# Optimization experiments

Measured on AMD Instinct MI355X. Metric: run time of the kernel, lower is better.

Reference implementation:

```python
import jax, jax.numpy as jnp
import numpy as np

BUCKET_SIZE = 128
HEADS = 8
HEAD_DIM = 64
LOOK_BACKWARD = 1
LOOK_FORWARD = 0  # causal => no look forward
TOKEN_SELF_ATTN_VALUE = -50000.0


def look_around(x, backward, forward, pad_value):
    n = x.shape[1]
    pw = [(0, 0)] * x.ndim
    pw[1] = (backward, forward)
    px = jnp.pad(x, pw, constant_values=pad_value)
    return jnp.concatenate([px[:, i:i + n] for i in range(backward + forward + 1)], axis=2)


def shift(x):
    # relative-shift trick: (..., i, j) -> (..., i, j)
    *lead, i, j = x.shape
    x = jnp.concatenate([x, jnp.zeros((*lead, i, i), x.dtype)], axis=-1)
    l = i + j - 1
    x = x.reshape(*lead, i * (i + j))
    pad = (-x.shape[-1]) % l
    x = jnp.concatenate([x, jnp.zeros((*lead, pad), x.dtype)], axis=-1)
    x = x.reshape(*lead, -1, l)
    return x[..., :i, i - 1:]


def setup_inputs() -> dict:
    key = jax.random.key(0)
    kq, kk, kv, kr = jax.random.split(key, 4)
    B, H, T, E = 2, HEADS, 8192, HEAD_DIM
    q = jax.random.normal(kq, (B, H, T, E), dtype=jnp.float32)
    k = jax.random.normal(kk, (B, H, T, E), dtype=jnp.float32)
    v = jax.random.normal(kv, (B, H, T, E), dtype=jnp.float32)
    rel_weights = jax.random.normal(kr, (2 * BUCKET_SIZE, H, E), dtype=jnp.float32)
    return {"q": q, "k": k, "v": v, "rel_weights": rel_weights}


def reference(q, k, v, rel_weights):
    B, H, T, E = q.shape
    qm = q.reshape(B * H, T, E)
    km = k.reshape(B * H, T, E)
    vm = v.reshape(B * H, T, E)

    # shared_qk: l2-normalize keys (F.normalize with eps=1e-12)
    km = km / jnp.maximum(jnp.linalg.norm(km, axis=-1, keepdims=True), 1e-12)

    buckets = T // BUCKET_SIZE
    bq = qm.reshape(B * H, buckets, BUCKET_SIZE, E)
    bk = km.reshape(B * H, buckets, BUCKET_SIZE, E)
    bv = vm.reshape(B * H, buckets, BUCKET_SIZE, E)

    bk = look_around(bk, LOOK_BACKWARD, LOOK_FORWARD, -1.0)
    bv = look_around(bv, LOOK_BACKWARD, LOOK_FORWARD, -1.0)

    ticker = jnp.arange(T, dtype=q.dtype)
    bq_t = ticker.reshape(1, buckets, BUCKET_SIZE)
    bq_k = look_around(bq_t, LOOK_BACKWARD, LOOK_FORWARD, -1.0)

    scale = E ** -0.5
    dots = jnp.einsum('bnie,bnje->bnij', bq, bk) * scale

    # relative positional bias
    bq5 = bq.reshape(B, H, buckets, BUCKET_SIZE, E)
    emb = jnp.einsum('bhnid,jhd->bhnij', bq5, rel_weights) * scale
    dots = dots + shift(emb).reshape(dots.shape)

    mask_value = -jnp.finfo(dots.dtype).max
    # shared_qk: mask self-attention positions
    self_mask = bq_t[:, :, :, None] == bq_k[:, :, None, :]
    dots = jnp.where(self_mask, TOKEN_SELF_ATTN_VALUE, dots)
    # causal mask
    causal_mask = bq_t[:, :, :, None] < bq_k[:, :, None, :]
    dots = jnp.where(causal_mask, mask_value, dots)
    # look-around padding mask
    pad_mask = (bq_k == -1.0)[:, :, None, :]
    dots = jnp.where(pad_mask, mask_value, dots)

    attn = jax.nn.softmax(dots, axis=-1)
    out = jnp.einsum('bnij,bnje->bnie', attn, bv)
    return out.reshape(B, H, T, E)
```

## Files before the change

kernel.cpp:

```cpp
#include <hip/hip_runtime.h>
#include <float.h>

#define NHEAD 8

typedef __attribute__((ext_vector_type(8))) short bf16x8;
typedef __attribute__((ext_vector_type(4))) float f32x4;

static __device__ __forceinline__ unsigned short bfbits(float f) {
    unsigned int u = __float_as_uint(f);
    u += 0x7fffu + ((u >> 16) & 1u);
    return (unsigned short)(u >> 16);
}
static __device__ __forceinline__ float bf2f_lo(unsigned int u) { return __uint_as_float(u << 16); }
static __device__ __forceinline__ float bf2f_hi(unsigned int u) { return __uint_as_float(u & 0xffff0000u); }

static __device__ __forceinline__ int swz64(int r, int c) {
    return (r << 6) + (c ^ ((r & 7) << 3));
}
static __device__ __forceinline__ int vIdx(int c, int kk) {
    return (c << 8) + (kk ^ ((c & 31) << 2));
}
static __device__ __forceinline__ int pIdx(int wv, int row, int col) {
    const int ch = (col >> 3) ^ (row & 3);
    return (wv * 16 + row) * 40 + ch * 8 + (col & 7);
}

static __device__ __forceinline__ f32x4 mfma16(bf16x8 a, bf16x8 b, f32x4 c) {
    return __builtin_amdgcn_mfma_f32_16x16x32_bf16(a, b, c, 0, 0, 0);
}

__global__ __launch_bounds__(512, 4)
void local_attn_kernel(const float* __restrict__ qg, const float* __restrict__ kg,
                       const float* __restrict__ vg, const float* __restrict__ rwg,
                       float* __restrict__ outg)
{
    __shared__ __align__(16) unsigned short sB[256 * 64];
    __shared__ __align__(16) unsigned short sV[64 * 256];
    __shared__ __align__(16) unsigned short sP[8 * 16 * 40];

    const int tid  = threadIdx.x;
    const int lane = tid & 63;
    const int wv   = tid >> 6;
    const int jl   = lane & 15;
    const int hi   = lane >> 4;

    const int lb = ((blockIdx.x & 7) << 7) + (blockIdx.x >> 3);
    const int bh = lb >> 6;
    const int n  = lb & 63;
    const int h  = bh & 7;

    const float scale = 0.125f;

    const float* Qp = qg + ((size_t)bh * 8192 + (size_t)n * 128) * 64;
    const float* Kp = kg + (size_t)bh * 8192 * 64 + ((long)n - 1) * 128 * 64;
    const float* Vp = vg + (size_t)bh * 8192 * 64 + ((long)n - 1) * 128 * 64;

    const int cr = tid >> 4;
    const int c0 = (tid & 15) << 2;

    #pragma unroll
    for (int pp = 0; pp < 8; ++pp) {
        const int row = pp * 32 + cr;
        f32x4 x = {0.f, 0.f, 0.f, 0.f};
        if (!(n == 0 && row < 128))
            x = *reinterpret_cast<const f32x4*>(Vp + row * 64 + c0);
        #pragma unroll
        for (int q = 0; q < 4; ++q)
            sV[vIdx(c0 + q, row)] = bfbits(x[q]);
    }

    const int arow = wv * 16 + jl;
    const int kq0  = hi << 3;
    const float* qr = Qp + arow * 64 + kq0;
    const f32x4 qa = *reinterpret_cast<const f32x4*>(qr);
    const f32x4 qb = *reinterpret_cast<const f32x4*>(qr + 4);
    const f32x4 qc = *reinterpret_cast<const f32x4*>(qr + 32);
    const f32x4 qd = *reinterpret_cast<const f32x4*>(qr + 36);
    bf16x8 aq0, aq1;
    #pragma unroll
    for (int q = 0; q < 4; ++q) {
        aq0[q]     = (short)bfbits(qa[q] * scale);
        aq0[q + 4] = (short)bfbits(qb[q] * scale);
        aq1[q]     = (short)bfbits(qc[q] * scale);
        aq1[q + 4] = (short)bfbits(qd[q] * scale);
    }

    #pragma unroll
    for (int pp = 0; pp < 8; ++pp) {
        const int row = pp * 32 + cr;
        const f32x4 x = *reinterpret_cast<const f32x4*>(rwg + ((size_t)row * NHEAD + h) * 64 + c0);
        ushort4 pk = make_ushort4(bfbits(x[0]), bfbits(x[1]), bfbits(x[2]), bfbits(x[3]));
        *reinterpret_cast<ushort4*>(&sB[swz64(row, c0)]) = pk;
    }

    f32x4 kreg[8];
    #pragma unroll
    for (int pp = 0; pp < 8; ++pp) {
        const int row = pp * 32 + cr;
        if (n == 0 && row < 128) kreg[pp] = f32x4{0.f, 0.f, 0.f, 0.f};
        else kreg[pp] = *reinterpret_cast<const f32x4*>(Kp + row * 64 + c0);
    }

    __syncthreads();

    const int ibase = wv * 16 + (hi << 2);

    unsigned int e01[17], e23[17];
    #pragma unroll
    for (int s = 0; s < 17; ++s) {
        unsigned int p01 = 0, p23 = 0;
        const int ts = s + 7 - wv;
        if (ts >= 0 && ts < 16) {
            const int rr = ts * 16 + jl;
            const bf16x8 b0 = *reinterpret_cast<const bf16x8*>(&sB[swz64(rr, kq0)]);
            const bf16x8 b1 = *reinterpret_cast<const bf16x8*>(&sB[swz64(rr, 32 + kq0)]);
            f32x4 e = {0.f, 0.f, 0.f, 0.f};
            e = mfma16(aq0, b0, e);
            e = mfma16(aq1, b1, e);
            p01 = (unsigned int)bfbits(e[0]) | ((unsigned int)bfbits(e[1]) << 16);
            p23 = (unsigned int)bfbits(e[2]) | ((unsigned int)bfbits(e[3]) << 16);
        }
        e01[s] = p01; e23[s] = p23;
    }

    __syncthreads();

    #pragma unroll
    for (int pp = 0; pp < 8; ++pp) {
        const int row = pp * 32 + cr;
        const f32x4 x = kreg[pp];
        float ss = x[0] * x[0] + x[1] * x[1] + x[2] * x[2] + x[3] * x[3];
        ss += __shfl_xor(ss, 1);
        ss += __shfl_xor(ss, 2);
        ss += __shfl_xor(ss, 4);
        ss += __shfl_xor(ss, 8);
        const float rn = 1.0f / fmaxf(sqrtf(ss), 1e-12f);
        ushort4 pk = make_ushort4(bfbits(x[0] * rn), bfbits(x[1] * rn),
                                  bfbits(x[2] * rn), bfbits(x[3] * rn));
        *reinterpret_cast<ushort4*>(&sB[swz64(row, c0)]) = pk;
    }

    __syncthreads();

    const int tMax = wv + 8;
    const int cv0 = 4 * hi + 1, cv1 = 4 * hi + 2, cv2 = 4 * hi + 3, cv3 = 4 * hi + 4;
    const int sl0 = (hi << 4) | ((jl - cv0) & 15);
    const int sl1 = (hi << 4) | ((jl - cv1) & 15);
    const int sl2 = (hi << 4) | ((jl - cv2) & 15);
    const int sl3 = (hi << 4) | ((jl - cv3) & 15);
    const bool g0 = jl >= cv0, g1 = jl >= cv1, g2 = jl >= cv2, g3 = jl >= cv3;

    unsigned int lo0 = (unsigned int)__shfl((int)e01[0], sl0);
    unsigned int lo1 = (unsigned int)__shfl((int)e01[0], sl1);
    unsigned int lo2 = (unsigned int)__shfl((int)e23[0], sl2);
    unsigned int lo3 = (unsigned int)__shfl((int)e23[0], sl3);

    f32x4 dots[16] = {};
    #pragma unroll
    for (int t = 0; t < 16; ++t) {
        if (t <= tMax) {
            const unsigned int h0 = (unsigned int)__shfl((int)e01[t + 1], sl0);
            const unsigned int h1 = (unsigned int)__shfl((int)e01[t + 1], sl1);
            const unsigned int h2 = (unsigned int)__shfl((int)e23[t + 1], sl2);
            const unsigned int h3 = (unsigned int)__shfl((int)e23[t + 1], sl3);
            const int rr = t * 16 + jl;
            const bf16x8 b0 = *reinterpret_cast<const bf16x8*>(&sB[swz64(rr, kq0)]);
            const bf16x8 b1 = *reinterpret_cast<const bf16x8*>(&sB[swz64(rr, 32 + kq0)]);
            f32x4 d = {0.f, 0.f, 0.f, 0.f};
            d = mfma16(aq0, b0, d);
            d = mfma16(aq1, b1, d);
            const float bias[4] = { bf2f_lo(g0 ? h0 : lo0), bf2f_hi(g1 ? h1 : lo1),
                                    bf2f_lo(g2 ? h2 : lo2), bf2f_hi(g3 ? h3 : lo3) };
            #pragma unroll
            for (int r = 0; r < 4; ++r) {
                const int i  = ibase + r;
                const int dd = rr - i;
                float x = d[r] + bias[r];
                x = (dd == 128) ? -50000.0f : x;
                x = (dd > 128) ? -3.0e38f : x;
                if (n == 0) x = (rr < 128) ? -3.0e38f : x;
                d[r] = x;
            }
            dots[t] = d;
            lo0 = h0; lo1 = h1; lo2 = h2; lo3 = h3;
        }
    }

    float mx[4] = {-3.0e38f, -3.0e38f, -3.0e38f, -3.0e38f};
    #pragma unroll
    for (int t = 0; t < 16; ++t) {
        if (t <= tMax) {
            #pragma unroll
            for (int r = 0; r < 4; ++r) mx[r] = fmaxf(mx[r], dots[t][r]);
        }
    }
    #pragma unroll
    for (int r = 0; r < 4; ++r) {
        mx[r] = fmaxf(mx[r], __shfl_xor(mx[r], 1));
        mx[r] = fmaxf(mx[r], __shfl_xor(mx[r], 2));
        mx[r] = fmaxf(mx[r], __shfl_xor(mx[r], 4));
        mx[r] = fmaxf(mx[r], __shfl_xor(mx[r], 8));
    }
    float sm[4] = {0.f, 0.f, 0.f, 0.f};
    #pragma unroll
    for (int t = 0; t < 16; ++t) {
        if (t <= tMax) {
            #pragma unroll
            for (int r = 0; r < 4; ++r) {
                const float pe = __expf(dots[t][r] - mx[r]);
                dots[t][r] = pe;
                sm[r] += pe;
            }
        }
    }
    float rinv[4];
    #pragma unroll
    for (int r = 0; r < 4; ++r) {
        sm[r] += __shfl_xor(sm[r], 1);
        sm[r] += __shfl_xor(sm[r], 2);
        sm[r] += __shfl_xor(sm[r], 4);
        sm[r] += __shfl_xor(sm[r], 8);
        rinv[r] = 1.0f / sm[r];
    }

    f32x4 o[4] = {};
    #pragma unroll
    for (int pv = 0; pv < 8; ++pv) {
        if (2 * pv <= tMax) {
            #pragma unroll
            for (int tt = 0; tt < 2; ++tt) {
                const int t = 2 * pv + tt;
                #pragma unroll
                for (int r = 0; r < 4; ++r) {
                    unsigned short val = 0;
                    if (t <= tMax) val = bfbits(dots[t][r]);
                    sP[pIdx(wv, 4 * hi + r, tt * 16 + jl)] = val;
                }
            }
            const bf16x8 pa = *reinterpret_cast<const bf16x8*>(&sP[pIdx(wv, jl, kq0)]);
            #pragma unroll
            for (int ct = 0; ct < 4; ++ct) {
                const int c = ct * 16 + jl;
                const ushort4 v0 = *reinterpret_cast<const ushort4*>(&sV[vIdx(c, pv * 32 + kq0)]);
                const ushort4 v1 = *reinterpret_cast<const ushort4*>(&sV[vIdx(c, pv * 32 + kq0 + 4)]);
                bf16x8 vb;
                vb[0] = (short)v0.x; vb[1] = (short)v0.y; vb[2] = (short)v0.z; vb[3] = (short)v0.w;
                vb[4] = (short)v1.x; vb[5] = (short)v1.y; vb[6] = (short)v1.z; vb[7] = (short)v1.w;
                o[ct] = mfma16(pa, vb, o[ct]);
            }
        }
    }

    float* Op = outg + ((size_t)bh * 8192 + (size_t)n * 128) * 64;
    #pragma unroll
    for (int ct = 0; ct < 4; ++ct)
        #pragma unroll
        for (int r = 0; r < 4; ++r)
            Op[(ibase + r) * 64 + ct * 16 + jl] = o[ct][r] * rinv[r];
}

extern "C" void kernel_launch(void* const* d_in, const int* in_sizes, int n_in,
                              void* d_out, int out_size, void* d_ws, size_t ws_size,
                              hipStream_t stream) {
    const float* q  = (const float*)d_in[0];
    const float* k  = (const float*)d_in[1];
    const float* v  = (const float*)d_in[2];
    const float* rw = (const float*)d_in[3];
    float* out = (float*)d_out;
    local_attn_kernel<<<dim3(1024), dim3(512), 0, stream>>>(q, k, v, rw, out);
}
```

Measured before the change: 59.68 us.

## Reorder phases: compute QK first, then interleave rel-bias MFMA with shifts

The kernel now normalizes K into shared memory first and computes the QK dot products before loading the relative-position weights. The relative-bias MFMAs are computed on the fly inside the masking loop rather than stored in two 17-entry register arrays. The f32 K register staging array is replaced by a smaller packed bf16 rel-weight array. It also switches to the library bf16 conversion intrinsic and uses a bit_cast to build V fragments, cutting register pressure and conversion ALU work at the cost of restructured phase ordering.

```diff
diff --git a/kernel.cpp b/kernel.cpp
--- a/kernel.cpp
+++ b/kernel.cpp
@@ -1,4 +1,5 @@
 #include <hip/hip_runtime.h>
+#include <hip/hip_bf16.h>
 #include <float.h>
 
 #define NHEAD 8
@@ -6,10 +7,14 @@
 typedef __attribute__((ext_vector_type(8))) short bf16x8;
 typedef __attribute__((ext_vector_type(4))) float f32x4;
 
-static __device__ __forceinline__ unsigned short bfbits(float f) {
-    unsigned int u = __float_as_uint(f);
-    u += 0x7fffu + ((u >> 16) & 1u);
-    return (unsigned short)(u >> 16);
+struct US44 { ushort4 a, b; };
+
+static __device__ __forceinline__ unsigned short bfb(float f) {
+    __hip_bfloat16 h = __float2bfloat16(f);
+    unsigned short u; __builtin_memcpy(&u, &h, 2); return u;
+}
+static __device__ __forceinline__ unsigned int pk2(float a, float b) {
+    return (unsigned int)bfb(a) | ((unsigned int)bfb(b) << 16);
 }
 static __device__ __forceinline__ float bf2f_lo(unsigned int u) { return __uint_as_float(u << 16); }
 static __device__ __forceinline__ float bf2f_hi(unsigned int u) { return __uint_as_float(u & 0xffff0000u); }
@@ -66,8 +71,36 @@
             x = *reinterpret_cast<const f32x4*>(Vp + row * 64 + c0);
         #pragma unroll
         for (int q = 0; q < 4; ++q)
-            sV[vIdx(c0 + q, row)] = bfbits(x[q]);
-    }
+            sV[vIdx(c0 + q, row)] = bfb(x[q]);
+    }
+
+    #pragma unroll
+    for (int pp = 0; pp < 8; ++pp) {
+        const int row = pp * 32 + cr;
+        f32x4 x = {0.f, 0.f, 0.f, 0.f};
+        if (!(n == 0 && row < 128))
+            x = *reinterpret_cast<const f32x4*>(Kp + row * 64 + c0);
+        float ss = x[0] * x[0] + x[1] * x[1] + x[2] * x[2] + x[3] * x[3];
+        ss += __shfl_xor(ss, 1);
+        ss += __shfl_xor(ss, 2);
+        ss += __shfl_xor(ss, 4);
+        ss += __shfl_xor(ss, 8);
+        const float rn = 1.0f / fmaxf(sqrtf(ss), 1e-12f);
+        ushort4 pkk = make_ushort4(bfb(x[0] * rn), bfb(x[1] * rn),
+                                   bfb(x[2] * rn), bfb(x[3] * rn));
+        *reinterpret_cast<ushort4*>(&sB[swz64(row, c0)]) = pkk;
+    }
+
+    uint2 rwu[8];
+    #pragma unroll
+    for (int pp = 0; pp < 8; ++pp) {
+        const int row = pp * 32 + cr;
+        const f32x4 x = *reinterpret_cast<const f32x4*>(rwg + ((size_t)row * NHEAD + h) * 64 + c0);
+        rwu[pp] = make_uint2(pk2(x[0], x[1]), pk2(x[2], x[3]));
+    }
+    #pragma unroll
+    for (int pp = 0; pp < 8; ++pp)
+        asm volatile("" :: "v"(rwu[pp].x), "v"(rwu[pp].y));
 
     const int arow = wv * 16 + jl;
     const int kq0  = hi << 3;
@@ -79,48 +112,29 @@
     bf16x8 aq0, aq1;
     #pragma unroll
     for (int q = 0; q < 4; ++q) {
-        aq0[q]     = (short)bfbits(qa[q] * scale);
-        aq0[q + 4] = (short)bfbits(qb[q] * scale);
-        aq1[q]     = (short)bfbits(qc[q] * scale);
-        aq1[q + 4] = (short)bfbits(qd[q] * scale);
-    }
-
-    #pragma unroll
-    for (int pp = 0; pp < 8; ++pp) {
-        const int row = pp * 32 + cr;
-        const f32x4 x = *reinterpret_cast<const f32x4*>(rwg + ((size_t)row * NHEAD + h) * 64 + c0);
-        ushort4 pk = make_ushort4(bfbits(x[0]), bfbits(x[1]), bfbits(x[2]), bfbits(x[3]));
-        *reinterpret_cast<ushort4*>(&sB[swz64(row, c0)]) = pk;
-    }
-
-    f32x4 kreg[8];
-    #pragma unroll
-    for (int pp = 0; pp < 8; ++pp) {
-        const int row = pp * 32 + cr;
-        if (n == 0 && row < 128) kreg[pp] = f32x4{0.f, 0.f, 0.f, 0.f};
-        else kreg[pp] = *reinterpret_cast<const f32x4*>(Kp + row * 64 + c0);
+        aq0[q]     = (short)bfb(qa[q] * scale);
+        aq0[q + 4] = (short)bfb(qb[q] * scale);
+        aq1[q]     = (short)bfb(qc[q] * scale);
+        aq1[q + 4] = (short)bfb(qd[q] * scale);
     }
 
     __syncthreads();
 
     const int ibase = wv * 16 + (hi << 2);
-
-    unsigned int e01[17], e23[17];
-    #pragma unroll
-    for (int s = 0; s < 17; ++s) {
-        unsigned int p01 = 0, p23 = 0;
-        const int ts = s + 7 - wv;
-        if (ts >= 0 && ts < 16) {
-            const int rr = ts * 16 + jl;
+    const int tMax  = wv + 8;
+
+    f32x4 dots[16] = {};
+    #pragma unroll
+    for (int t = 0; t < 16; ++t) {
+        if (t <= tMax) {
+            const int rr = t * 16 + jl;
             const bf16x8 b0 = *reinterpret_cast<const bf16x8*>(&sB[swz64(rr, kq0)]);
             const bf16x8 b1 = *reinterpret_cast<const bf16x8*>(&sB[swz64(rr, 32 + kq0)]);
-            f32x4 e = {0.f, 0.f, 0.f, 0.f};
-            e = mfma16(aq0, b0, e);
-            e = mfma16(aq1, b1, e);
-            p01 = (unsigned int)bfbits(e[0]) | ((unsigned int)bfbits(e[1]) << 16);
-            p23 = (unsigned int)bfbits(e[2]) | ((unsigned int)bfbits(e[3]) << 16);
-        }
-        e01[s] = p01; e23[s] = p23;
+            f32x4 d = {0.f, 0.f, 0.f, 0.f};
+            d = mfma16(aq0, b0, d);
+            d = mfma16(aq1, b1, d);
+            dots[t] = d;
+        }
     }
 
     __syncthreads();
@@ -128,21 +142,11 @@
     #pragma unroll
     for (int pp = 0; pp < 8; ++pp) {
         const int row = pp * 32 + cr;
-        const f32x4 x = kreg[pp];
-        float ss = x[0] * x[0] + x[1] * x[1] + x[2] * x[2] + x[3] * x[3];
-        ss += __shfl_xor(ss, 1);
-        ss += __shfl_xor(ss, 2);
-        ss += __shfl_xor(ss, 4);
-        ss += __shfl_xor(ss, 8);
-        const float rn = 1.0f / fmaxf(sqrtf(ss), 1e-12f);
-        ushort4 pk = make_ushort4(bfbits(x[0] * rn), bfbits(x[1] * rn),
-                                  bfbits(x[2] * rn), bfbits(x[3] * rn));
-        *reinterpret_cast<ushort4*>(&sB[swz64(row, c0)]) = pk;
+        *reinterpret_cast<uint2*>(&sB[swz64(row, c0)]) = rwu[pp];
     }
 
     __syncthreads();
 
-    const int tMax = wv + 8;
     const int cv0 = 4 * hi + 1, cv1 = 4 * hi + 2, cv2 = 4 * hi + 3, cv3 = 4 * hi + 4;
     const int sl0 = (hi << 4) | ((jl - cv0) & 15);
     const int sl1 = (hi << 4) | ((jl - cv1) & 15);
@@ -150,38 +154,54 @@
     const int sl3 = (hi << 4) | ((jl - cv3) & 15);
     const bool g0 = jl >= cv0, g1 = jl >= cv1, g2 = jl >= cv2, g3 = jl >= cv3;
 
-    unsigned int lo0 = (unsigned int)__shfl((int)e01[0], sl0);
-    unsigned int lo1 = (unsigned int)__shfl((int)e01[0], sl1);
-    unsigned int lo2 = (unsigned int)__shfl((int)e23[0], sl2);
-    unsigned int lo3 = (unsigned int)__shfl((int)e23[0], sl3);
-
-    f32x4 dots[16] = {};
-    #pragma unroll
-    for (int t = 0; t < 16; ++t) {
-        if (t <= tMax) {
-            const unsigned int h0 = (unsigned int)__shfl((int)e01[t + 1], sl0);
-            const unsigned int h1 = (unsigned int)__shfl((int)e01[t + 1], sl1);
-            const unsigned int h2 = (unsigned int)__shfl((int)e23[t + 1], sl2);
-            const unsigned int h3 = (unsigned int)__shfl((int)e23[t + 1], sl3);
-            const int rr = t * 16 + jl;
-            const bf16x8 b0 = *reinterpret_cast<const bf16x8*>(&sB[swz64(rr, kq0)]);
-            const bf16x8 b1 = *reinterpret_cast<const bf16x8*>(&sB[swz64(rr, 32 + kq0)]);
-            f32x4 d = {0.f, 0.f, 0.f, 0.f};
-            d = mfma16(aq0, b0, d);
-            d = mfma16(aq1, b1, d);
+    unsigned int cur01, cur23;
+    {
+        const int rr = (7 - wv) * 16 + jl;
+        const bf16x8 b0 = *reinterpret_cast<const bf16x8*>(&sB[swz64(rr, kq0)]);
+        const bf16x8 b1 = *reinterpret_cast<const bf16x8*>(&sB[swz64(rr, 32 + kq0)]);
+        f32x4 e = {0.f, 0.f, 0.f, 0.f};
+        e = mfma16(aq0, b0, e);
+        e = mfma16(aq1, b1, e);
+        cur01 = pk2(e[0], e[1]);
+        cur23 = pk2(e[2], e[3]);
+    }
+    unsigned int lo0 = (unsigned int)__shfl((int)cur01, sl0);
+    unsigned int lo1 = (unsigned int)__shfl((int)cur01, sl1);
+    unsigned int lo2 = (unsigned int)__shfl((int)cur23, sl2);
+    unsigned int lo3 = (unsigned int)__shfl((int)cur23, sl3);
+
+    #pragma unroll
+    for (int t = 0; t < 16; ++t) {
+        if (t <= tMax) {
+            unsigned int n01 = 0, n23 = 0;
+            const int ts = t + 8 - wv;
+            if (ts < 16) {
+                const int rr = ts * 16 + jl;
+                const bf16x8 b0 = *reinterpret_cast<const bf16x8*>(&sB[swz64(rr, kq0)]);
+                const bf16x8 b1 = *reinterpret_cast<const bf16x8*>(&sB[swz64(rr, 32 + kq0)]);
+                f32x4 e = {0.f, 0.f, 0.f, 0.f};
+                e = mfma16(aq0, b0, e);
+                e = mfma16(aq1, b1, e);
+                n01 = pk2(e[0], e[1]);
+                n23 = pk2(e[2], e[3]);
+            }
+            const unsigned int h0 = (unsigned int)__shfl((int)n01, sl0);
+            const unsigned int h1 = (unsigned int)__shfl((int)n01, sl1);
+            const unsigned int h2 = (unsigned int)__shfl((int)n23, sl2);
+            const unsigned int h3 = (unsigned int)__shfl((int)n23, sl3);
             const float bias[4] = { bf2f_lo(g0 ? h0 : lo0), bf2f_hi(g1 ? h1 : lo1),
                                     bf2f_lo(g2 ? h2 : lo2), bf2f_hi(g3 ? h3 : lo3) };
+            const int rr2 = t * 16 + jl;
             #pragma unroll
             for (int r = 0; r < 4; ++r) {
                 const int i  = ibase + r;
-                const int dd = rr - i;
-                float x = d[r] + bias[r];
+                const int dd = rr2 - i;
+                float x = dots[t][r] + bias[r];
                 x = (dd == 128) ? -50000.0f : x;
                 x = (dd > 128) ? -3.0e38f : x;
-                if (n == 0) x = (rr < 128) ? -3.0e38f : x;
-                d[r] = x;
-            }
-            dots[t] = d;
+                if (n == 0) x = (rr2 < 128) ? -3.0e38f : x;
+                dots[t][r] = x;
+            }
             lo0 = h0; lo1 = h1; lo2 = h2; lo3 = h3;
         }
     }
@@ -233,7 +253,7 @@
                 #pragma unroll
                 for (int r = 0; r < 4; ++r) {
                     unsigned short val = 0;
-                    if (t <= tMax) val = bfbits(dots[t][r]);
+                    if (t <= tMax) val = bfb(dots[t][r]);
                     sP[pIdx(wv, 4 * hi + r, tt * 16 + jl)] = val;
                 }
             }
@@ -243,9 +263,7 @@
                 const int c = ct * 16 + jl;
                 const ushort4 v0 = *reinterpret_cast<const ushort4*>(&sV[vIdx(c, pv * 32 + kq0)]);
                 const ushort4 v1 = *reinterpret_cast<const ushort4*>(&sV[vIdx(c, pv * 32 + kq0 + 4)]);
-                bf16x8 vb;
-                vb[0] = (short)v0.x; vb[1] = (short)v0.y; vb[2] = (short)v0.z; vb[3] = (short)v0.w;
-                vb[4] = (short)v1.x; vb[5] = (short)v1.y; vb[6] = (short)v1.z; vb[7] = (short)v1.w;
+                const bf16x8 vb = __builtin_bit_cast(bf16x8, US44{v0, v1});
                 o[ct] = mfma16(pa, vb, o[ct]);
             }
         }
```

New measurement: 52.76 us. 11.6% less time.
